# Optimization experiments

Measured on AMD Instinct MI355X. Metric: run time of the kernel, lower is better.

The kernel has to match this reference:

```python
import jax, jax.numpy as jnp
import numpy as np

B, S, D = 8, 2048, 512

def setup_inputs() -> dict:
    key = jax.random.key(0)
    k1, k2, k3 = jax.random.split(key, 3)
    context = jax.random.normal(k1, (B, S, D), dtype=jnp.float32)
    # nn.Linear default init ~ U(-1/sqrt(D), 1/sqrt(D)); scale keeps softmax sane
    bound = 1.0 / np.sqrt(D)
    W_in = jax.random.uniform(k2, (D, D), dtype=jnp.float32, minval=-bound, maxval=bound)
    W_out = jax.random.uniform(k3, (D, D), dtype=jnp.float32, minval=-bound, maxval=bound)
    return {"context": context, "W_in": W_in, "W_out": W_out}

def reference(context, W_in, W_out):
    # linear_in: x @ W_in.T (torch Linear convention)
    c = jnp.einsum('bsd,ed->bse', context, W_in)            # [B,S,D]
    scores = jnp.einsum('bsd,btd->bst', c, c)               # [B,S,S], no 1/sqrt(d) scale
    attn = jax.nn.softmax(scores, axis=-1)                  # [B,S,S]
    ctx = jnp.einsum('bst,btd->bsd', attn, c)               # [B,S,D]
    out = jnp.einsum('bsd,ed->bse', jnp.tanh(ctx), W_out)   # linear_out
    return out, attn
```

## Files before the change

### kernel.cpp

```cpp
#include <hip/hip_runtime.h>
#include <cstdint>
#include <cstddef>

#define Bc 8
#define Sc 2048
#define Dc 512

typedef float f32x4 __attribute__((ext_vector_type(4)));
typedef __bf16 bf16x8 __attribute__((ext_vector_type(8)));
typedef __bf16 bf16x4 __attribute__((ext_vector_type(4)));

__device__ __forceinline__ void gload_lds16(const void* g, void* l) {
    __builtin_amdgcn_global_load_lds((const __attribute__((address_space(1))) void*)g,
                                     (__attribute__((address_space(3))) void*)l, 16, 0, 0);
}

__device__ __forceinline__ f32x4 mfma16x16x32(bf16x8 a, bf16x8 b, f32x4 c) {
    return __builtin_amdgcn_mfma_f32_16x16x32_bf16(a, b, c, 0, 0, 0);
}

__global__ void k_convert_w(const float* __restrict__ wi, const float* __restrict__ wo,
                            __bf16* __restrict__ wib, __bf16* __restrict__ wob) {
    int i = blockIdx.x * 256 + threadIdx.x;
    wib[i] = (__bf16)wi[i];
    wob[i] = (__bf16)wo[i];
}

__global__ __launch_bounds__(256) void k_scores(
        const __bf16* __restrict__ c, __bf16* __restrict__ Ebuf,
        float2* __restrict__ stats)
{
    __shared__ alignas(16) char smem[34816];
    __bf16* As = (__bf16*)smem;
    __bf16* Bs = (__bf16*)(smem + 16384);
    const int tid  = threadIdx.x;
    const int wave = tid >> 6, lane = tid & 63;
    const int waveM = wave >> 1, waveN = wave & 1;
    const int bid  = blockIdx.x;
    const int bz   = bid & 7;
    const int col0 = ((bid >> 3) & 15) * 128;
    const int row0 = (bid >> 7) * 128;
    const __bf16* A  = c + (size_t)bz * Sc * Dc;

    f32x4 acc[4][4] = {};

    for (int k0 = 0; k0 < Dc; k0 += 64) {
        #pragma unroll
        for (int i = 0; i < 4; ++i) {
            int flat = i * 2048 + wave * 512 + lane * 8;
            int r  = flat >> 6;
            int cc = (flat >> 3) & 7;
            int gc = (cc ^ (r & 7)) << 3;
            gload_lds16(A + (size_t)(row0 + r) * Dc + k0 + gc, As + i * 2048 + wave * 512);
            gload_lds16(A + (size_t)(col0 + r) * Dc + k0 + gc, Bs + i * 2048 + wave * 512);
        }
        __syncthreads();
        #pragma unroll
        for (int ks = 0; ks < 2; ++ks) {
            const int kc = ks * 4 + (lane >> 4);
            bf16x8 av[4], bv[4];
            #pragma unroll
            for (int mi = 0; mi < 4; ++mi) {
                int r = waveM * 64 + mi * 16 + (lane & 15);
                av[mi] = *(const bf16x8*)&As[r * 64 + ((kc ^ (r & 7)) << 3)];
            }
            #pragma unroll
            for (int ni = 0; ni < 4; ++ni) {
                int r = waveN * 64 + ni * 16 + (lane & 15);
                bv[ni] = *(const bf16x8*)&Bs[r * 64 + ((kc ^ (r & 7)) << 3)];
            }
            #pragma unroll
            for (int mi = 0; mi < 4; ++mi)
                #pragma unroll
                for (int ni = 0; ni < 4; ++ni)
                    acc[mi][ni] = mfma16x16x32(av[mi], bv[ni], acc[mi][ni]);
        }
        __syncthreads();
    }

    const int rb = (lane >> 4) << 2;
    const int cb = lane & 15;
    __bf16* Es = (__bf16*)smem;
    #pragma unroll
    for (int mi = 0; mi < 4; ++mi)
        #pragma unroll
        for (int rr = 0; rr < 4; ++rr) {
            float mx = fmaxf(fmaxf(acc[mi][0][rr], acc[mi][1][rr]),
                             fmaxf(acc[mi][2][rr], acc[mi][3][rr]));
            #pragma unroll
            for (int off = 1; off < 16; off <<= 1) mx = fmaxf(mx, __shfl_xor(mx, off));
            const int rloc = waveM * 64 + mi * 16 + rb + rr;
            float zs = 0.f;
            #pragma unroll
            for (int ni = 0; ni < 4; ++ni) {
                float e = __expf(acc[mi][ni][rr] - mx);
                zs += e;
                Es[rloc * 136 + waveN * 64 + ni * 16 + cb] = (__bf16)e;
            }
            #pragma unroll
            for (int off = 1; off < 16; off <<= 1) zs += __shfl_xor(zs, off);
            if ((lane & 15) == 0)
                stats[((size_t)bz * Sc + row0 + rloc) * 32 + (col0 >> 6) + waveN] =
                    make_float2(mx, zs);
        }
    __syncthreads();
    #pragma unroll
    for (int p = 0; p < 8; ++p) {
        int r  = p * 16 + (tid >> 4);
        int cc = (tid & 15) * 8;
        bf16x8 v = *(const bf16x8*)&Es[r * 136 + cc];
        *(bf16x8*)&Ebuf[((size_t)bz * Sc + row0 + r) * Sc + col0 + cc] = v;
    }
}

__global__ __launch_bounds__(256) void k_combine(const float2* __restrict__ stats,
                                                 float* __restrict__ corrTab) {
    int r = blockIdx.x * 256 + threadIdx.x;
    float2 s[32];
    #pragma unroll
    for (int i = 0; i < 32; ++i) s[i] = stats[(size_t)r * 32 + i];
    float M = s[0].x;
    #pragma unroll
    for (int i = 1; i < 32; ++i) M = fmaxf(M, s[i].x);
    float Z = 0.f;
    #pragma unroll
    for (int i = 0; i < 32; ++i) Z += s[i].y * __expf(s[i].x - M);
    float zi = 1.f / Z;
    #pragma unroll
    for (int i = 0; i < 32; ++i) corrTab[(size_t)r * 32 + i] = __expf(s[i].x - M) * zi;
}

__global__ __launch_bounds__(512) void k_pv_fused(
        const __bf16* __restrict__ Ebuf,
        const __bf16* __restrict__ cT,
        const float* __restrict__ corrTab,
        float* __restrict__ attn,
        __bf16* __restrict__ ctx)
{
    __shared__ alignas(16) __bf16 As[64 * 64];
    __shared__ alignas(16) __bf16 Bs[512 * 64];
    const int tid  = threadIdx.x;
    const int wave = tid >> 6, lane = tid & 63;
    const int b    = blockIdx.x & 7;
    const int row0 = (blockIdx.x >> 3) * 64;
    const __bf16* Bt = cT + (size_t)b * Dc * Sc;

    const int ar = tid >> 3;
    const int ac = (tid & 7) * 8;
    const __bf16* erow = Ebuf + ((size_t)b * Sc + row0 + ar) * Sc + ac;
    const float*  crow = corrTab + ((size_t)b * Sc + row0 + ar) * 32;
    float*        prow = attn + ((size_t)b * Sc + row0 + ar) * Sc + ac;
    const int a_addr = ar * 64 + (((ac >> 3) ^ (ar & 7)) << 3);

    f32x4 acc[4][4] = {};
    const int NT = Sc / 64;

    auto stageB = [&](int kt) {
        #pragma unroll
        for (int i = 0; i < 8; ++i) {
            int chunk = i * 512 + tid;
            int r  = chunk >> 3;
            int cc = chunk & 7;
            gload_lds16(Bt + (size_t)r * Sc + kt + ((cc ^ (r & 7)) << 3),
                        Bs + (size_t)chunk * 8);
        }
    };

    bf16x8 e = *(const bf16x8*)&erow[0];
    float  cf = crow[0];
    f32x4 p0, p1;
    #pragma unroll
    for (int j = 0; j < 4; ++j) { p0[j] = (float)e[j] * cf; p1[j] = (float)e[4 + j] * cf; }
    {
        bf16x8 pb;
        #pragma unroll
        for (int j = 0; j < 4; ++j) { pb[j] = (__bf16)p0[j]; pb[4 + j] = (__bf16)p1[j]; }
        *(bf16x8*)&As[a_addr] = pb;
    }
    stageB(0);
    __builtin_amdgcn_sched_barrier(0);
    *(f32x4*)&prow[0] = p0;
    *(f32x4*)&prow[4] = p1;
    e  = *(const bf16x8*)&erow[64];
    cf = crow[1];
    asm volatile("s_waitcnt vmcnt(4) lgkmcnt(0)" ::: "memory");
    __builtin_amdgcn_sched_barrier(0);
    __builtin_amdgcn_s_barrier();

    for (int t = 0; t < NT; ++t) {
        bf16x8 av[4][2], bv[2][4];
        #pragma unroll
        for (int ks = 0; ks < 2; ++ks) {
            const int kc = ks * 4 + (lane >> 4);
            #pragma unroll
            for (int mi = 0; mi < 4; ++mi) {
                int r = mi * 16 + (lane & 15);
                av[mi][ks] = *(const bf16x8*)&As[r * 64 + ((kc ^ (r & 7)) << 3)];
            }
            #pragma unroll
            for (int ni = 0; ni < 4; ++ni) {
                int r = wave * 64 + ni * 16 + (lane & 15);
                bv[ks][ni] = *(const bf16x8*)&Bs[r * 64 + ((kc ^ (r & 7)) << 3)];
            }
        }
        asm volatile("s_waitcnt lgkmcnt(0)" ::: "memory");
        __builtin_amdgcn_sched_barrier(0);
        __builtin_amdgcn_s_barrier();

        if (t + 1 < NT) {
            stageB((t + 1) * 64);
            __builtin_amdgcn_sched_barrier(0);
            f32x4 q0, q1;
            #pragma unroll
            for (int j = 0; j < 4; ++j) {
                q0[j] = (float)e[j] * cf; q1[j] = (float)e[4 + j] * cf;
            }
            bf16x8 pb;
            #pragma unroll
            for (int j = 0; j < 4; ++j) { pb[j] = (__bf16)q0[j]; pb[4 + j] = (__bf16)q1[j]; }
            *(bf16x8*)&As[a_addr] = pb;
            *(f32x4*)&prow[(t + 1) * 64]     = q0;
            *(f32x4*)&prow[(t + 1) * 64 + 4] = q1;
            if (t + 2 < NT) {
                e  = *(const bf16x8*)&erow[(t + 2) * 64];
                cf = crow[t + 2];
            }
        }

        #pragma unroll
        for (int ks = 0; ks < 2; ++ks)
            #pragma unroll
            for (int mi = 0; mi < 4; ++mi)
                #pragma unroll
                for (int ni = 0; ni < 4; ++ni)
                    acc[mi][ni] = mfma16x16x32(av[mi][ks], bv[ks][ni], acc[mi][ni]);

        if (t + 1 < NT) {
            if (t + 2 < NT)
                asm volatile("s_waitcnt vmcnt(4) lgkmcnt(0)" ::: "memory");
            else
                asm volatile("s_waitcnt vmcnt(2) lgkmcnt(0)" ::: "memory");
            __builtin_amdgcn_sched_barrier(0);
            __builtin_amdgcn_s_barrier();
        }
    }

    const int rb = (lane >> 4) << 2;
    const int cb = lane & 15;
    #pragma unroll
    for (int mi = 0; mi < 4; ++mi)
        #pragma unroll
        for (int ni = 0; ni < 4; ++ni) {
            int gr = row0 + mi * 16 + rb;
            int gc = wave * 64 + ni * 16 + cb;
            #pragma unroll
            for (int rr = 0; rr < 4; ++rr)
                ctx[(size_t)(b * Sc + gr + rr) * Dc + gc] = (__bf16)tanhf(acc[mi][ni][rr]);
        }
}

__global__ __launch_bounds__(256) void k_gemm_bf16(
        const __bf16* __restrict__ A, const __bf16* __restrict__ Bt,
        float* __restrict__ C, int lda, int ldb, int ldc, int K)
{
    __shared__ alignas(16) __bf16 smem[2 * 128 * 64];
    __bf16* As = smem;
    __bf16* Bs = smem + 128 * 64;
    const int tid  = threadIdx.x;
    const int wave = tid >> 6, lane = tid & 63;
    const int waveM = wave >> 1, waveN = wave & 1;
    const int row0 = blockIdx.y * 128;
    const int col0 = blockIdx.x * 128;

    f32x4 acc[4][4] = {};

    for (int k0 = 0; k0 < K; k0 += 64) {
        #pragma unroll
        for (int i = 0; i < 4; ++i) {
            int flat = i * 2048 + wave * 512 + lane * 8;
            int r  = flat >> 6;
            int cc = (flat >> 3) & 7;
            int gc = (cc ^ (r & 7)) << 3;
            gload_lds16(A  + (size_t)(row0 + r) * lda + k0 + gc, As + i * 2048 + wave * 512);
            gload_lds16(Bt + (size_t)(col0 + r) * ldb + k0 + gc, Bs + i * 2048 + wave * 512);
        }
        __syncthreads();
        #pragma unroll
        for (int ks = 0; ks < 2; ++ks) {
            const int kc = ks * 4 + (lane >> 4);
            bf16x8 av[4], bv[4];
            #pragma unroll
            for (int mi = 0; mi < 4; ++mi) {
                int r = waveM * 64 + mi * 16 + (lane & 15);
                av[mi] = *(const bf16x8*)&As[r * 64 + ((kc ^ (r & 7)) << 3)];
            }
            #pragma unroll
            for (int ni = 0; ni < 4; ++ni) {
                int r = waveN * 64 + ni * 16 + (lane & 15);
                bv[ni] = *(const bf16x8*)&Bs[r * 64 + ((kc ^ (r & 7)) << 3)];
            }
            #pragma unroll
            for (int mi = 0; mi < 4; ++mi)
                #pragma unroll
                for (int ni = 0; ni < 4; ++ni)
                    acc[mi][ni] = mfma16x16x32(av[mi], bv[ni], acc[mi][ni]);
        }
        __syncthreads();
    }

    const int rb = (lane >> 4) << 2;
    const int cb = lane & 15;
    #pragma unroll
    for (int mi = 0; mi < 4; ++mi)
        #pragma unroll
        for (int ni = 0; ni < 4; ++ni) {
            int gr = row0 + waveM * 64 + mi * 16 + rb;
            int gc = col0 + waveN * 64 + ni * 16 + cb;
            #pragma unroll
            for (int rr = 0; rr < 4; ++rr)
                C[(size_t)(gr + rr) * ldc + gc] = acc[mi][ni][rr];
        }
}

__global__ __launch_bounds__(256) void k_cproj(
        const float* __restrict__ A, const __bf16* __restrict__ Bt,
        __bf16* __restrict__ Cb, __bf16* __restrict__ CTb)
{
    __shared__ alignas(16) char smem[49152];
    float*  Asf = (float*)smem;
    __bf16* Bs  = (__bf16*)(smem + 32768);
    const int tid  = threadIdx.x;
    const int wave = tid >> 6, lane = tid & 63;
    const int waveM = wave >> 1, waveN = wave & 1;
    const int row0 = blockIdx.y * 128;
    const int col0 = blockIdx.x * 128;

    f32x4 acc[4][4] = {};

    for (int k0 = 0; k0 < Dc; k0 += 64) {
        #pragma unroll
        for (int i = 0; i < 8; ++i) {
            int flat = i * 1024 + wave * 256 + lane * 4;
            int r  = flat >> 6;
            int cc = (flat >> 2) & 15;
            int gc = (cc ^ (r & 15)) << 2;
            gload_lds16(A + (size_t)(row0 + r) * Dc + k0 + gc, Asf + i * 1024 + wave * 256);
        }
        #pragma unroll
        for (int i = 0; i < 4; ++i) {
            int flat = i * 2048 + wave * 512 + lane * 8;
            int r  = flat >> 6;
            int cc = (flat >> 3) & 7;
            int gc = (cc ^ (r & 7)) << 3;
            gload_lds16(Bt + (size_t)(col0 + r) * Dc + k0 + gc, Bs + i * 2048 + wave * 512);
        }
        __syncthreads();
        #pragma unroll
        for (int ks = 0; ks < 2; ++ks) {
            const int kc8 = ks * 4 + (lane >> 4);
            const int kc4 = kc8 << 1;
            bf16x8 av[4], bv[4];
            #pragma unroll
            for (int mi = 0; mi < 4; ++mi) {
                int r  = waveM * 64 + mi * 16 + (lane & 15);
                int r4 = r & 15;
                f32x4 lo = *(const f32x4*)&Asf[r * 64 + (((kc4    ) ^ r4) << 2)];
                f32x4 hi = *(const f32x4*)&Asf[r * 64 + (((kc4 + 1) ^ r4) << 2)];
                bf16x8 a;
                a[0] = (__bf16)lo[0]; a[1] = (__bf16)lo[1]; a[2] = (__bf16)lo[2]; a[3] = (__bf16)lo[3];
                a[4] = (__bf16)hi[0]; a[5] = (__bf16)hi[1]; a[6] = (__bf16)hi[2]; a[7] = (__bf16)hi[3];
                av[mi] = a;
            }
            #pragma unroll
            for (int ni = 0; ni < 4; ++ni) {
                int r = waveN * 64 + ni * 16 + (lane & 15);
                bv[ni] = *(const bf16x8*)&Bs[r * 64 + ((kc8 ^ (r & 7)) << 3)];
            }
            #pragma unroll
            for (int mi = 0; mi < 4; ++mi)
                #pragma unroll
                for (int ni = 0; ni < 4; ++ni)
                    acc[mi][ni] = mfma16x16x32(av[mi], bv[ni], acc[mi][ni]);
        }
        __syncthreads();
    }

    const int rb = (lane >> 4) << 2;
    const int cb = lane & 15;
    __bf16* T = (__bf16*)smem;
    #pragma unroll
    for (int mi = 0; mi < 4; ++mi)
        #pragma unroll
        for (int ni = 0; ni < 4; ++ni) {
            int lr = waveM * 64 + mi * 16 + rb;
            int lc = waveN * 64 + ni * 16 + cb;
            #pragma unroll
            for (int rr = 0; rr < 4; ++rr) {
                __bf16 h = (__bf16)acc[mi][ni][rr];
                Cb[(size_t)(row0 + lr + rr) * Dc + col0 + lc] = h;
                T[lc * 136 + lr + rr] = h;
            }
        }
    __syncthreads();
    const int bb = row0 >> 11;
    const int s0 = row0 & 2047;
    #pragma unroll
    for (int i = 0; i < 8; ++i) {
        int n  = i * 16 + (tid >> 4);
        int mo = (tid & 15) * 8;
        bf16x8 v = *(const bf16x8*)&T[n * 136 + mo];
        *(bf16x8*)&CTb[(size_t)bb * Dc * Sc + (size_t)(col0 + n) * Sc + s0 + mo] = v;
    }
}

extern "C" void kernel_launch(void* const* d_in, const int* in_sizes, int n_in,
                              void* d_out, int out_size, void* d_ws, size_t ws_size,
                              hipStream_t stream)
{
    (void)in_sizes; (void)n_in; (void)out_size; (void)ws_size;
    const float* context = (const float*)d_in[0];
    const float* W_in    = (const float*)d_in[1];
    const float* W_out   = (const float*)d_in[2];
    float* out  = (float*)d_out;
    float* attn = out + (size_t)Bc * Sc * Dc;

    char* ws = (char*)d_ws;
    __bf16* c_bf    = (__bf16*)ws;
    __bf16* cT_bf   = (__bf16*)(ws + 16777216);
    __bf16* wi_bf   = (__bf16*)(ws + 33554432);
    __bf16* wo_bf   = (__bf16*)(ws + 34078720);
    float2* stats   = (float2*)(ws + 34603008);
    float*  corrTab = (float*)(ws + 38797312);
    __bf16* Ebuf    = (__bf16*)(ws + 40894464);

    k_convert_w<<<dim3(Dc * Dc / 256), 256, 0, stream>>>(W_in, W_out, wi_bf, wo_bf);

    k_cproj<<<dim3(Dc / 128, (Bc * Sc) / 128), 256, 0, stream>>>(context, wi_bf, c_bf, cT_bf);

    k_scores<<<dim3(Bc * 16 * 16), 256, 0, stream>>>(c_bf, Ebuf, stats);

    k_combine<<<dim3(Bc * Sc / 256), 256, 0, stream>>>(stats, corrTab);

    k_pv_fused<<<dim3((Sc / 64) * Bc), 512, 0, stream>>>(Ebuf, cT_bf, corrTab, attn, c_bf);

    k_gemm_bf16<<<dim3(Dc / 128, (Bc * Sc) / 128, 1), 256, 0, stream>>>(
        c_bf, wo_bf, out, Dc, Dc, Dc, Dc);
}
```

Baseline: 185.4 us.

## Double-buffer LDS tiles in scores kernel to overlap global loads with MFMA

The scores GEMM now uses two LDS buffers. While MFMAs run on the current k-tile, the next tile is fetched into the other buffer with direct global-to-LDS loads, and one explicit vmcnt wait plus barrier replaces the previous pair of syncthreads per iteration. This is meant to hide global memory latency behind compute. LDS use grows to 64KB per block, which may reduce occupancy, and the whole A/B fragment set is held in registers before the MFMAs, which raises register pressure.

```diff
diff --git a/kernel.cpp b/kernel.cpp
--- a/kernel.cpp
+++ b/kernel.cpp
@@ -30,9 +30,7 @@
         const __bf16* __restrict__ c, __bf16* __restrict__ Ebuf,
         float2* __restrict__ stats)
 {
-    __shared__ alignas(16) char smem[34816];
-    __bf16* As = (__bf16*)smem;
-    __bf16* Bs = (__bf16*)(smem + 16384);
+    __shared__ alignas(16) char smem[65536];
     const int tid  = threadIdx.x;
     const int wave = tid >> 6, lane = tid & 63;
     const int waveM = wave >> 1, waveN = wave & 1;
@@ -44,7 +42,9 @@
 
     f32x4 acc[4][4] = {};
 
-    for (int k0 = 0; k0 < Dc; k0 += 64) {
+    auto stage = [&](char* buf, int k0) {
+        __bf16* As = (__bf16*)buf;
+        __bf16* Bs = (__bf16*)(buf + 16384);
         #pragma unroll
         for (int i = 0; i < 4; ++i) {
             int flat = i * 2048 + wave * 512 + lane * 8;
@@ -54,28 +54,52 @@
             gload_lds16(A + (size_t)(row0 + r) * Dc + k0 + gc, As + i * 2048 + wave * 512);
             gload_lds16(A + (size_t)(col0 + r) * Dc + k0 + gc, Bs + i * 2048 + wave * 512);
         }
-        __syncthreads();
+    };
+
+    stage(smem, 0);
+    asm volatile("s_waitcnt vmcnt(0)" ::: "memory");
+    __builtin_amdgcn_sched_barrier(0);
+    __builtin_amdgcn_s_barrier();
+    __builtin_amdgcn_sched_barrier(0);
+
+    #pragma unroll
+    for (int t = 0; t < 8; ++t) {
+        char* cur = smem + ((t & 1) ? 32768 : 0);
+        char* nxt = smem + ((t & 1) ? 0 : 32768);
+        __bf16* As = (__bf16*)cur;
+        __bf16* Bs = (__bf16*)(cur + 16384);
+        bf16x8 av[4][2], bv[2][4];
         #pragma unroll
         for (int ks = 0; ks < 2; ++ks) {
             const int kc = ks * 4 + (lane >> 4);
-            bf16x8 av[4], bv[4];
             #pragma unroll
             for (int mi = 0; mi < 4; ++mi) {
                 int r = waveM * 64 + mi * 16 + (lane & 15);
-                av[mi] = *(const bf16x8*)&As[r * 64 + ((kc ^ (r & 7)) << 3)];
+                av[mi][ks] = *(const bf16x8*)&As[r * 64 + ((kc ^ (r & 7)) << 3)];
             }
             #pragma unroll
             for (int ni = 0; ni < 4; ++ni) {
                 int r = waveN * 64 + ni * 16 + (lane & 15);
-                bv[ni] = *(const bf16x8*)&Bs[r * 64 + ((kc ^ (r & 7)) << 3)];
-            }
+                bv[ks][ni] = *(const bf16x8*)&Bs[r * 64 + ((kc ^ (r & 7)) << 3)];
+            }
+        }
+        if (t + 1 < 8) {
+            stage(nxt, (t + 1) * 64);
+            __builtin_amdgcn_sched_barrier(0);
+        }
+        #pragma unroll
+        for (int ks = 0; ks < 2; ++ks)
             #pragma unroll
             for (int mi = 0; mi < 4; ++mi)
                 #pragma unroll
                 for (int ni = 0; ni < 4; ++ni)
-                    acc[mi][ni] = mfma16x16x32(av[mi], bv[ni], acc[mi][ni]);
-        }
-        __syncthreads();
+                    acc[mi][ni] = mfma16x16x32(av[mi][ks], bv[ks][ni], acc[mi][ni]);
+        if (t + 1 < 8) {
+            asm volatile("s_waitcnt vmcnt(0)" ::: "memory");
+            __builtin_amdgcn_sched_barrier(0);
+            __builtin_amdgcn_s_barrier();
+            __builtin_amdgcn_sched_barrier(0);
+        }
     }
 
     const int rb = (lane >> 4) << 2;
```

Result: no change. 187.7 us (+1.2%).
